# Kernel tuning notes

Measured on AMD Instinct MI355X. Metric: run time of the kernel, lower is better.

The kernel has to match this reference:

```python
import jax, jax.numpy as jnp
import numpy as np

N_NODES = 50000
N_EDGES = 800000
QRY = 128
KEY = 128
VAL = 128
HEADS = 8
HEAD_FEATS = VAL // HEADS
BN_EPS = 1e-5


def setup_inputs() -> dict:
    key = jax.random.key(0)
    ks = jax.random.split(key, 12)
    inp = {
        "ft_q": jax.random.normal(ks[0], (N_NODES, QRY), dtype=jnp.float32),
        "ft_k": jax.random.normal(ks[1], (N_NODES, KEY), dtype=jnp.float32),
        "src": jax.random.randint(ks[2], (N_EDGES,), 0, N_NODES, dtype=jnp.int32),
        "dst": jax.random.randint(ks[3], (N_EDGES,), 0, N_NODES, dtype=jnp.int32),
        # learned params
        "Wq": jax.random.normal(ks[4], (VAL, QRY), dtype=jnp.float32) / np.sqrt(QRY),
        "bq": jnp.zeros((VAL,), dtype=jnp.float32),
        "Wk": jax.random.normal(ks[5], (VAL, KEY), dtype=jnp.float32) / np.sqrt(KEY),
        "Wv": jax.random.normal(ks[6], (VAL, QRY), dtype=jnp.float32) / np.sqrt(QRY),
        "attn_e": jax.random.normal(ks[7], (VAL,), dtype=jnp.float32),
        "bn_q_g": jnp.ones((QRY,), dtype=jnp.float32),
        "bn_q_b": jnp.zeros((QRY,), dtype=jnp.float32),
        "bn_k_g": jnp.ones((KEY,), dtype=jnp.float32),
        "bn_k_b": jnp.zeros((KEY,), dtype=jnp.float32),
    }
    return inp


def _batch_norm(x, gamma, beta):
    # training-mode BatchNorm1d: normalize over batch dim
    mean = jnp.mean(x, axis=0, keepdims=True)
    var = jnp.var(x, axis=0, keepdims=True)
    return (x - mean) * jax.lax.rsqrt(var + BN_EPS) * gamma + beta


def reference(ft_q, ft_k, src, dst, Wq, bq, Wk, Wv, attn_e,
              bn_q_g, bn_q_b, bn_k_g, bn_k_b):
    ft_q = _batch_norm(ft_q, bn_q_g, bn_q_b)
    ft_k = _batch_norm(ft_k, bn_k_g, bn_k_b)

    q = ft_q @ Wq.T + bq                      # [N, VAL]
    k = ft_k @ Wk.T                           # [N, VAL]
    v = (ft_q @ Wv.T).reshape(-1, HEADS, HEAD_FEATS)  # [N, H, D]

    # u_add_v: per-edge e = q[src] + k[dst]
    e = q[src] + k[dst]                       # [E, VAL]
    e = (attn_e * jax.nn.sigmoid(e)).reshape(-1, HEADS, HEAD_FEATS).sum(-1)  # [E, H]

    # edge_softmax grouped by destination node
    m = jax.ops.segment_max(e, dst, num_segments=N_NODES)   # [N, H]
    ex = jnp.exp(e - m[dst])                                # [E, H]
    s = jax.ops.segment_sum(ex, dst, num_segments=N_NODES)  # [N, H]
    a = ex / s[dst]                                         # [E, H]

    # u_mul_e_sum: scatter-sum of v[src] * a over destination
    msg = v[src] * a[:, :, None]                            # [E, H, D]
    rst = jax.ops.segment_sum(msg, dst, num_segments=N_NODES)  # [N, H, D]
    return rst.reshape(-1, VAL)
```

## Files before the change

### kernel.cpp

```cpp
#include <hip/hip_runtime.h>

#define N_NODES 50000
#define N_EDGES 800000
#define FEATS 128
#define NCHUNK 196
#define CPAD 50176
#define GEMM_BX 196
#define GEMM_BLOCKS 588
#define SCAT_BLOCKS 3125
#define NTILE 782
#define NF_WAVES 8192

typedef __attribute__((ext_vector_type(8))) short bf16x8;
typedef __attribute__((ext_vector_type(4))) float f32x4;

__device__ __forceinline__ unsigned short f2bf(float f){
  unsigned u = __float_as_uint(f);
  u += 0x7FFF + ((u >> 16) & 1);
  return (unsigned short)(u >> 16);
}
__device__ __forceinline__ void unpack8(uint4 p, float* f){
  f[0]=__uint_as_float(p.x << 16); f[1]=__uint_as_float(p.x & 0xffff0000u);
  f[2]=__uint_as_float(p.y << 16); f[3]=__uint_as_float(p.y & 0xffff0000u);
  f[4]=__uint_as_float(p.z << 16); f[5]=__uint_as_float(p.z & 0xffff0000u);
  f[6]=__uint_as_float(p.w << 16); f[7]=__uint_as_float(p.w & 0xffff0000u);
}

__global__ __launch_bounds__(256) void stats_hist_kernel(
    const float* __restrict__ ftq, const float* __restrict__ ftk,
    float* __restrict__ sums, const int* __restrict__ dstE,
    int* __restrict__ counts, int* __restrict__ csums){
  __shared__ float red[4*FEATS];
  __shared__ int lchunk[NCHUNK];
  int tid = threadIdx.x, bid = blockIdx.x;
  if (bid < 768){
    for (int i = tid; i < 4*FEATS; i += 256) red[i] = 0.f;
    __syncthreads();
    int c = tid & 127, half = tid >> 7;
    float sq=0.f, qq=0.f, sk=0.f, kk2=0.f;
    for (int r = bid*2 + half; r < N_NODES; r += 1536){
      float xq = ftq[(size_t)r*FEATS + c];
      float xk = ftk[(size_t)r*FEATS + c];
      sq += xq; qq += xq*xq; sk += xk; kk2 += xk*xk;
    }
    atomicAdd(&red[0*FEATS+c], sq);
    atomicAdd(&red[1*FEATS+c], qq);
    atomicAdd(&red[2*FEATS+c], sk);
    atomicAdd(&red[3*FEATS+c], kk2);
    __syncthreads();
    if (tid < FEATS){
      atomicAdd(&sums[0*FEATS+tid], red[0*FEATS+tid]);
      atomicAdd(&sums[1*FEATS+tid], red[1*FEATS+tid]);
      atomicAdd(&sums[2*FEATS+tid], red[2*FEATS+tid]);
      atomicAdd(&sums[3*FEATS+tid], red[3*FEATS+tid]);
    }
  } else {
    for (int i = tid; i < NCHUNK; i += 256) lchunk[i] = 0;
    __syncthreads();
    for (int t = (bid-768)*256 + tid; t < N_EDGES; t += 256*256){
      int d = dstE[t];
      atomicAdd(&counts[d], 1);
      atomicAdd(&lchunk[d >> 8], 1);
    }
    __syncthreads();
    for (int i = tid; i < NCHUNK; i += 256)
      if (lchunk[i]) atomicAdd(&csums[i], lchunk[i]);
  }
}

__global__ __launch_bounds__(256) void scan_fold_kernel(
    const int* __restrict__ counts, const int* __restrict__ csums,
    int* __restrict__ loc, int* __restrict__ bscan,
    const float* __restrict__ Wq, const float* __restrict__ bq,
    const float* __restrict__ Wk, const float* __restrict__ Wv,
    const float* __restrict__ gq, const float* __restrict__ bqn,
    const float* __restrict__ gk, const float* __restrict__ bkn,
    const float* __restrict__ sums,
    unsigned short* __restrict__ Wb, float* __restrict__ bias){
  __shared__ int s[256];
  int tid = threadIdx.x, bid = blockIdx.x;
  if (bid < NCHUNK){
    int i = bid*256 + tid;
    int v = counts[i];
    s[tid] = v; __syncthreads();
    for (int d = 1; d < 256; d <<= 1){
      int tv = (tid >= d) ? s[tid-d] : 0; __syncthreads();
      s[tid] += tv; __syncthreads();
    }
    loc[i] = s[tid] - v;
  } else if (bid == NCHUNK){
    int v = (tid < NCHUNK) ? csums[tid] : 0;
    s[tid] = v; __syncthreads();
    for (int d = 1; d < 256; d <<= 1){
      int tv = (tid >= d) ? s[tid-d] : 0; __syncthreads();
      s[tid] += tv; __syncthreads();
    }
    if (tid < NCHUNK) bscan[tid] = s[tid] - v;
  } else {
    int wv = (bid - NCHUNK - 1)*4 + (tid >> 6);
    int lane = tid & 63;
    int m = wv >> 7;
    int o = wv & 127;
    const float* Wsrc = (m==0) ? Wq : (m==1) ? Wv : Wk;
    const float* g   = (m==2) ? gk : gq;
    const float* bb  = (m==2) ? bkn : bqn;
    const float* s0  = (m==2) ? (sums + 2*FEATS) : sums;
    const float invN = 1.0f / (float)N_NODES;
    float acc = 0.f;
    unsigned short w2[2];
    int i0 = lane*2;
    #pragma unroll
    for (int t = 0; t < 2; t++){
      int i = i0 + t;
      float mean = s0[i]*invN;
      float var  = s0[FEATS+i]*invN - mean*mean;
      float rstd = rsqrtf(var + 1e-5f);
      float scale = g[i]*rstd;
      float shift = bb[i] - mean*scale;
      float w = Wsrc[o*FEATS + i];
      w2[t] = f2bf(w*scale);
      acc += shift*w;
    }
    ((unsigned*)Wb)[(m*FEATS*FEATS + o*FEATS + i0) >> 1] =
        (unsigned)w2[0] | ((unsigned)w2[1] << 16);
    #pragma unroll
    for (int off = 1; off < 64; off <<= 1) acc += __shfl_xor(acc, off);
    if (lane == 0) bias[m*FEATS + o] = acc + ((m==0) ? bq[o] : 0.f);
  }
}

__global__ __launch_bounds__(256) void gemm_scatter_kernel(
    const float* __restrict__ ftq, const float* __restrict__ ftk,
    const unsigned short* __restrict__ Wball, const float* __restrict__ biasall,
    unsigned short* __restrict__ qv, unsigned short* __restrict__ kb,
    const int* __restrict__ dstE, const int* __restrict__ srcE,
    const int* __restrict__ loc, const int* __restrict__ bscan,
    int* __restrict__ cursor, int* __restrict__ src_csr){
  __shared__ unsigned short Bs[FEATS][136];
  int tid = threadIdx.x, bid = blockIdx.x;
  if (bid >= GEMM_BLOCKS){
    int t = (bid - GEMM_BLOCKS)*256 + tid;
    int d = dstE[t];
    int p = atomicAdd(&cursor[d], 1);
    src_csr[loc[d] + bscan[d >> 8] + p] = srcE[t];
    return;
  }
  int m = bid / GEMM_BX;
  int bx = bid - m*GEMM_BX;
  const float* X = (m==2) ? ftk : ftq;
  {
    const uint4* srcp = (const uint4*)(Wball + m*FEATS*FEATS);
    for (int idx = tid; idx < FEATS*FEATS/8; idx += 256){
      int n = idx >> 4;
      int kk = (idx & 15) * 8;
      *(uint4*)&Bs[n][kk] = srcp[idx];
    }
  }
  __syncthreads();
  int wave = tid >> 6, lane = tid & 63;
  int mrow = lane & 15, quad = lane >> 4;
  unsigned short* Out = (m==2) ? kb : (qv + m*128);
  const int ostride = (m==2) ? FEATS : 256;
  float bv[8];
  #pragma unroll
  for (int ct = 0; ct < 8; ct++) bv[ct] = biasall[m*FEATS + ct*16 + mrow];
  for (int t = bx; t < NTILE; t += GEMM_BX){
    int row0 = t*64;
    int arow = row0 + wave*16 + mrow;
    bool rok = arow < N_NODES;
    size_t abase = (size_t)(rok ? arow : 0) * FEATS;
    bf16x8 afrag[4];
    #pragma unroll
    for (int kt = 0; kt < 4; kt++){
      const float* xp = X + abase + kt*32 + quad*8;
      float4 x0 = *(const float4*)xp;
      float4 x1 = *(const float4*)(xp + 4);
      if (!rok){ x0 = make_float4(0.f,0.f,0.f,0.f); x1 = x0; }
      bf16x8 a;
      a[0]=(short)f2bf(x0.x); a[1]=(short)f2bf(x0.y); a[2]=(short)f2bf(x0.z); a[3]=(short)f2bf(x0.w);
      a[4]=(short)f2bf(x1.x); a[5]=(short)f2bf(x1.y); a[6]=(short)f2bf(x1.z); a[7]=(short)f2bf(x1.w);
      afrag[kt] = a;
    }
    f32x4 acc[8];
    #pragma unroll
    for (int i = 0; i < 8; i++) acc[i] = (f32x4){0.f,0.f,0.f,0.f};
    #pragma unroll
    for (int kt = 0; kt < 4; kt++){
      int kbk = kt*32 + quad*8;
      #pragma unroll
      for (int ct = 0; ct < 8; ct++){
        bf16x8 b = *(bf16x8*)&Bs[ct*16 + mrow][kbk];
        acc[ct] = __builtin_amdgcn_mfma_f32_16x16x32_bf16(afrag[kt], b, acc[ct], 0, 0, 0);
      }
    }
    #pragma unroll
    for (int ct = 0; ct < 8; ct++){
      int col = ct*16 + mrow;
      #pragma unroll
      for (int v = 0; v < 4; v++){
        int orow = row0 + wave*16 + quad*4 + v;
        unsigned ub = f2bf(acc[ct][v] + bv[ct]);
        unsigned partner = (unsigned)__shfl_xor((int)ub, 1);
        if (!(mrow & 1) && orow < N_NODES)
          *(unsigned*)&Out[(size_t)orow*ostride + col] = ub | (partner << 16);
      }
    }
  }
}

__global__ __launch_bounds__(256) void node_fused_kernel(
    const unsigned short* __restrict__ qv, const unsigned short* __restrict__ kb,
    const float* __restrict__ attn, const int* __restrict__ src_csr,
    const int* __restrict__ loc, const int* __restrict__ bscan,
    float* __restrict__ out){
  int tid = threadIdx.x;
  int lane = tid & 63;
  int h = lane & 7, g = lane >> 3;
  int w = blockIdx.x*4 + (tid >> 6);
  const float L2E = 1.44269504f;
  float ar[16];
  {
    const uint4* ap = (const uint4*)(attn + h*16);
    uint4 a0 = ap[0], a1 = ap[1], a2 = ap[2], a3 = ap[3];
    ar[0]=__uint_as_float(a0.x); ar[1]=__uint_as_float(a0.y); ar[2]=__uint_as_float(a0.z); ar[3]=__uint_as_float(a0.w);
    ar[4]=__uint_as_float(a1.x); ar[5]=__uint_as_float(a1.y); ar[6]=__uint_as_float(a1.z); ar[7]=__uint_as_float(a1.w);
    ar[8]=__uint_as_float(a2.x); ar[9]=__uint_as_float(a2.y); ar[10]=__uint_as_float(a2.z); ar[11]=__uint_as_float(a2.w);
    ar[12]=__uint_as_float(a3.x); ar[13]=__uint_as_float(a3.y); ar[14]=__uint_as_float(a3.z); ar[15]=__uint_as_float(a3.w);
  }
  for (int n = w; n < N_NODES; n += NF_WAVES){
    int off0 = loc[n]   + bscan[n>>8];
    int off1 = loc[n+1] + bscan[(n+1)>>8];
    int deg = off1 - off0;
    if (deg == 0){
      ((float2*)(out + (size_t)n*FEATS))[lane] = make_float2(0.f, 0.f);
      continue;
    }
    float kf2[16];
    {
      const unsigned short* kr = kb + (size_t)n*FEATS + h*16;
      uint4 k0 = *(const uint4*)kr;
      uint4 k1 = *(const uint4*)(kr + 8);
      float kf[16]; unpack8(k0, kf); unpack8(k1, kf+8);
      #pragma unroll
      for (int i = 0; i < 16; i++) kf2[i] = -L2E * kf[i];
    }
    float ssum = 0.f;
    float acc[16];
    #pragma unroll
    for (int i = 0; i < 16; i++) acc[i] = 0.f;
    int s_next = (g < deg) ? src_csr[off0 + g] : 0;
    for (int j = g; j < deg; j += 8){
      int s = s_next;
      if (j + 8 < deg) s_next = src_csr[off0 + j + 8];
      const unsigned short* qr = qv + (size_t)s*256 + h*16;
      uint4 q0 = *(const uint4*)qr;
      uint4 q1 = *(const uint4*)(qr + 8);
      uint4 v0 = *(const uint4*)(qr + 128);
      uint4 v1 = *(const uint4*)(qr + 136);
      float qf[16]; unpack8(q0, qf); unpack8(q1, qf+8);
      float t = 0.f;
      #pragma unroll
      for (int i = 0; i < 16; i++){
        float xs = fmaf(qf[i], -L2E, kf2[i]);
        float sg = __builtin_amdgcn_rcpf(1.f + __builtin_amdgcn_exp2f(xs));
        t = fmaf(ar[i], sg, t);
      }
      float ex = __builtin_amdgcn_exp2f(t * L2E);
      ssum += ex;
      float vf[16]; unpack8(v0, vf); unpack8(v1, vf+8);
      #pragma unroll
      for (int i = 0; i < 16; i++) acc[i] = fmaf(ex, vf[i], acc[i]);
    }
    ssum += __shfl_xor(ssum, 8); ssum += __shfl_xor(ssum, 16); ssum += __shfl_xor(ssum, 32);
    #pragma unroll
    for (int i = 0; i < 16; i++){
      acc[i] += __shfl_xor(acc[i], 8);
      acc[i] += __shfl_xor(acc[i], 16);
      acc[i] += __shfl_xor(acc[i], 32);
    }
    if (g == 0){
      float inv_s = 1.f / ssum;
      float4* op = (float4*)(out + (size_t)n*FEATS + h*16);
      op[0] = make_float4(acc[0]*inv_s, acc[1]*inv_s, acc[2]*inv_s, acc[3]*inv_s);
      op[1] = make_float4(acc[4]*inv_s, acc[5]*inv_s, acc[6]*inv_s, acc[7]*inv_s);
      op[2] = make_float4(acc[8]*inv_s, acc[9]*inv_s, acc[10]*inv_s, acc[11]*inv_s);
      op[3] = make_float4(acc[12]*inv_s, acc[13]*inv_s, acc[14]*inv_s, acc[15]*inv_s);
    }
  }
}

extern "C" void kernel_launch(void* const* d_in, const int* in_sizes, int n_in,
                              void* d_out, int out_size, void* d_ws, size_t ws_size,
                              hipStream_t stream){
  (void)in_sizes; (void)n_in; (void)out_size; (void)ws_size;
  const float* ftq  = (const float*)d_in[0];
  const float* ftk  = (const float*)d_in[1];
  const int*   srcE = (const int*)d_in[2];
  const int*   dstE = (const int*)d_in[3];
  const float* Wq   = (const float*)d_in[4];
  const float* bq   = (const float*)d_in[5];
  const float* Wk   = (const float*)d_in[6];
  const float* Wv   = (const float*)d_in[7];
  const float* attn = (const float*)d_in[8];
  const float* gq   = (const float*)d_in[9];
  const float* bqn  = (const float*)d_in[10];
  const float* gk   = (const float*)d_in[11];
  const float* bkn  = (const float*)d_in[12];

  char* ws = (char*)d_ws;
  int*   counts  = (int*)(ws + 0);
  int*   cursor  = (int*)(ws + 200704);
  float* sums    = (float*)(ws + 400704);
  int*   csums   = (int*)(ws + 402752);
  int*   loc     = (int*)(ws + 403536);
  int*   bscan   = (int*)(ws + 604240);
  int*   src_csr = (int*)(ws + 605024);
  unsigned short* Wb = (unsigned short*)(ws + 3805024);
  float* biasf   = (float*)(ws + 3903328);
  unsigned short* qv = (unsigned short*)(ws + 3904864);
  unsigned short* kb = qv + (size_t)N_NODES*256;
  float* out = (float*)d_out;

  hipMemsetAsync(ws, 0, 403536, stream);

  hipLaunchKernelGGL(stats_hist_kernel, dim3(1024), dim3(256), 0, stream,
                     ftq, ftk, sums, dstE, counts, csums);
  hipLaunchKernelGGL(scan_fold_kernel, dim3(293), dim3(256), 0, stream,
                     counts, csums, loc, bscan,
                     Wq, bq, Wk, Wv, gq, bqn, gk, bkn, sums, Wb, biasf);
  hipLaunchKernelGGL(gemm_scatter_kernel, dim3(GEMM_BLOCKS + SCAT_BLOCKS), dim3(256), 0, stream,
                     ftq, ftk, Wb, biasf, qv, kb, dstE, srcE, loc, bscan, cursor, src_csr);
  hipLaunchKernelGGL(node_fused_kernel, dim3(NF_WAVES/4), dim3(256), 0, stream,
                     qv, kb, attn, src_csr, loc, bscan, out);
}
```

Baseline: 290.0 us.

## Merge CSR offsets, share A tiles across Q/V GEMMs, unroll edge loop by two

Each scan block now computes its chunk base itself from csums, giving a single global offsets array in place of loc and bscan plus a separate block scan. The Q and V projections now share one set of loaded and converted A fragments per tile, with the weight tile restaged in shared memory between them, so ft_q is read once for both. The node kernel processes two edges per lane per iteration, issuing both gathers together for more memory-level parallelism. This replaces the prefetch-next-index scheme and adds register pressure.

```diff
diff --git a/kernel.cpp b/kernel.cpp
--- a/kernel.cpp
+++ b/kernel.cpp
@@ -5,7 +5,8 @@
 #define FEATS 128
 #define NCHUNK 196
 #define CPAD 50176
-#define GEMM_BX 196
+#define GEMM_QV 392
+#define GEMM_K 196
 #define GEMM_BLOCKS 588
 #define SCAT_BLOCKS 3125
 #define NTILE 782
@@ -70,7 +71,7 @@
 
 __global__ __launch_bounds__(256) void scan_fold_kernel(
     const int* __restrict__ counts, const int* __restrict__ csums,
-    int* __restrict__ loc, int* __restrict__ bscan,
+    int* __restrict__ offsets,
     const float* __restrict__ Wq, const float* __restrict__ bq,
     const float* __restrict__ Wk, const float* __restrict__ Wv,
     const float* __restrict__ gq, const float* __restrict__ bqn,
@@ -78,8 +79,19 @@
     const float* __restrict__ sums,
     unsigned short* __restrict__ Wb, float* __restrict__ bias){
   __shared__ int s[256];
+  __shared__ int sbase;
   int tid = threadIdx.x, bid = blockIdx.x;
   if (bid < NCHUNK){
+    s[tid] = (tid < bid) ? csums[tid] : 0;
+    __syncthreads();
+    for (int d = 128; d > 0; d >>= 1){
+      if (tid < d) s[tid] += s[tid + d];
+      __syncthreads();
+    }
+    if (tid == 0) sbase = s[0];
+    __syncthreads();
+    int base = sbase;
+    __syncthreads();
     int i = bid*256 + tid;
     int v = counts[i];
     s[tid] = v; __syncthreads();
@@ -87,17 +99,9 @@
       int tv = (tid >= d) ? s[tid-d] : 0; __syncthreads();
       s[tid] += tv; __syncthreads();
     }
-    loc[i] = s[tid] - v;
-  } else if (bid == NCHUNK){
-    int v = (tid < NCHUNK) ? csums[tid] : 0;
-    s[tid] = v; __syncthreads();
-    for (int d = 1; d < 256; d <<= 1){
-      int tv = (tid >= d) ? s[tid-d] : 0; __syncthreads();
-      s[tid] += tv; __syncthreads();
-    }
-    if (tid < NCHUNK) bscan[tid] = s[tid] - v;
+    offsets[i] = base + s[tid] - v;
   } else {
-    int wv = (bid - NCHUNK - 1)*4 + (tid >> 6);
+    int wv = (bid - NCHUNK)*4 + (tid >> 6);
     int lane = tid & 63;
     int m = wv >> 7;
     int o = wv & 127;
@@ -134,42 +138,26 @@
     const unsigned short* __restrict__ Wball, const float* __restrict__ biasall,
     unsigned short* __restrict__ qv, unsigned short* __restrict__ kb,
     const int* __restrict__ dstE, const int* __restrict__ srcE,
-    const int* __restrict__ loc, const int* __restrict__ bscan,
-    int* __restrict__ cursor, int* __restrict__ src_csr){
+    const int* __restrict__ offsets, int* __restrict__ cursor,
+    int* __restrict__ src_csr){
   __shared__ unsigned short Bs[FEATS][136];
   int tid = threadIdx.x, bid = blockIdx.x;
   if (bid >= GEMM_BLOCKS){
     int t = (bid - GEMM_BLOCKS)*256 + tid;
     int d = dstE[t];
     int p = atomicAdd(&cursor[d], 1);
-    src_csr[loc[d] + bscan[d >> 8] + p] = srcE[t];
+    src_csr[offsets[d] + p] = srcE[t];
     return;
   }
-  int m = bid / GEMM_BX;
-  int bx = bid - m*GEMM_BX;
-  const float* X = (m==2) ? ftk : ftq;
-  {
-    const uint4* srcp = (const uint4*)(Wball + m*FEATS*FEATS);
-    for (int idx = tid; idx < FEATS*FEATS/8; idx += 256){
-      int n = idx >> 4;
-      int kk = (idx & 15) * 8;
-      *(uint4*)&Bs[n][kk] = srcp[idx];
-    }
-  }
-  __syncthreads();
   int wave = tid >> 6, lane = tid & 63;
   int mrow = lane & 15, quad = lane >> 4;
-  unsigned short* Out = (m==2) ? kb : (qv + m*128);
-  const int ostride = (m==2) ? FEATS : 256;
-  float bv[8];
-  #pragma unroll
-  for (int ct = 0; ct < 8; ct++) bv[ct] = biasall[m*FEATS + ct*16 + mrow];
-  for (int t = bx; t < NTILE; t += GEMM_BX){
+
+  auto loadA = [&](int t, bf16x8* af){
     int row0 = t*64;
     int arow = row0 + wave*16 + mrow;
     bool rok = arow < N_NODES;
+    const float* X = (bid < GEMM_QV) ? ftq : ftk;
     size_t abase = (size_t)(rok ? arow : 0) * FEATS;
-    bf16x8 afrag[4];
     #pragma unroll
     for (int kt = 0; kt < 4; kt++){
       const float* xp = X + abase + kt*32 + quad*8;
@@ -179,8 +167,18 @@
       bf16x8 a;
       a[0]=(short)f2bf(x0.x); a[1]=(short)f2bf(x0.y); a[2]=(short)f2bf(x0.z); a[3]=(short)f2bf(x0.w);
       a[4]=(short)f2bf(x1.x); a[5]=(short)f2bf(x1.y); a[6]=(short)f2bf(x1.z); a[7]=(short)f2bf(x1.w);
-      afrag[kt] = a;
-    }
+      af[kt] = a;
+    }
+  };
+  auto stageB = [&](int m){
+    const uint4* srcp = (const uint4*)(Wball + m*FEATS*FEATS);
+    for (int idx = tid; idx < FEATS*FEATS/8; idx += 256){
+      int n = idx >> 4;
+      int kk = (idx & 15) * 8;
+      *(uint4*)&Bs[n][kk] = srcp[idx];
+    }
+  };
+  auto compute_store = [&](int t, const bf16x8* af, int m){
     f32x4 acc[8];
     #pragma unroll
     for (int i = 0; i < 8; i++) acc[i] = (f32x4){0.f,0.f,0.f,0.f};
@@ -190,29 +188,56 @@
       #pragma unroll
       for (int ct = 0; ct < 8; ct++){
         bf16x8 b = *(bf16x8*)&Bs[ct*16 + mrow][kbk];
-        acc[ct] = __builtin_amdgcn_mfma_f32_16x16x32_bf16(afrag[kt], b, acc[ct], 0, 0, 0);
+        acc[ct] = __builtin_amdgcn_mfma_f32_16x16x32_bf16(af[kt], b, acc[ct], 0, 0, 0);
       }
     }
+    unsigned short* Out = (m==2) ? kb : (qv + m*128);
+    const int ostride = (m==2) ? FEATS : 256;
+    int row0 = t*64;
     #pragma unroll
     for (int ct = 0; ct < 8; ct++){
       int col = ct*16 + mrow;
+      float bv = biasall[m*FEATS + col];
       #pragma unroll
       for (int v = 0; v < 4; v++){
         int orow = row0 + wave*16 + quad*4 + v;
-        unsigned ub = f2bf(acc[ct][v] + bv[ct]);
+        unsigned ub = f2bf(acc[ct][v] + bv);
         unsigned partner = (unsigned)__shfl_xor((int)ub, 1);
         if (!(mrow & 1) && orow < N_NODES)
           *(unsigned*)&Out[(size_t)orow*ostride + col] = ub | (partner << 16);
       }
     }
+  };
+
+  if (bid < GEMM_QV){
+    int t0 = bid, t1 = bid + GEMM_QV;
+    bf16x8 a0[4], a1[4];
+    stageB(0);
+    loadA(t0, a0); loadA(t1, a1);
+    __syncthreads();
+    compute_store(t0, a0, 0);
+    compute_store(t1, a1, 0);
+    __syncthreads();
+    stageB(1);
+    __syncthreads();
+    compute_store(t0, a0, 1);
+    compute_store(t1, a1, 1);
+  } else {
+    int bx = bid - GEMM_QV;
+    stageB(2);
+    __syncthreads();
+    bf16x8 af[4];
+    for (int t = bx; t < NTILE; t += GEMM_K){
+      loadA(t, af);
+      compute_store(t, af, 2);
+    }
   }
 }
 
 __global__ __launch_bounds__(256) void node_fused_kernel(
     const unsigned short* __restrict__ qv, const unsigned short* __restrict__ kb,
     const float* __restrict__ attn, const int* __restrict__ src_csr,
-    const int* __restrict__ loc, const int* __restrict__ bscan,
-    float* __restrict__ out){
+    const int* __restrict__ offsets, float* __restrict__ out){
   int tid = threadIdx.x;
   int lane = tid & 63;
   int h = lane & 7, g = lane >> 3;
@@ -228,9 +253,8 @@
     ar[12]=__uint_as_float(a3.x); ar[13]=__uint_as_float(a3.y); ar[14]=__uint_as_float(a3.z); ar[15]=__uint_as_float(a3.w);
   }
   for (int n = w; n < N_NODES; n += NF_WAVES){
-    int off0 = loc[n]   + bscan[n>>8];
-    int off1 = loc[n+1] + bscan[(n+1)>>8];
-    int deg = off1 - off0;
+    int off0 = offsets[n];
+    int deg = offsets[n+1] - off0;
     if (deg == 0){
       ((float2*)(out + (size_t)n*FEATS))[lane] = make_float2(0.f, 0.f);
       continue;
@@ -248,28 +272,45 @@
     float acc[16];
     #pragma unroll
     for (int i = 0; i < 16; i++) acc[i] = 0.f;
-    int s_next = (g < deg) ? src_csr[off0 + g] : 0;
-    for (int j = g; j < deg; j += 8){
-      int s = s_next;
-      if (j + 8 < deg) s_next = src_csr[off0 + j + 8];
-      const unsigned short* qr = qv + (size_t)s*256 + h*16;
-      uint4 q0 = *(const uint4*)qr;
-      uint4 q1 = *(const uint4*)(qr + 8);
-      uint4 v0 = *(const uint4*)(qr + 128);
-      uint4 v1 = *(const uint4*)(qr + 136);
-      float qf[16]; unpack8(q0, qf); unpack8(q1, qf+8);
-      float t = 0.f;
+    for (int j = g; j < deg; j += 16){
+      int j2 = j + 8;
+      bool has2 = j2 < deg;
+      int s1 = src_csr[off0 + j];
+      int s2 = has2 ? src_csr[off0 + j2] : s1;
+      const unsigned short* qr1 = qv + (size_t)s1*256 + h*16;
+      const unsigned short* qr2 = qv + (size_t)s2*256 + h*16;
+      uint4 q10 = *(const uint4*)qr1;
+      uint4 q11 = *(const uint4*)(qr1 + 8);
+      uint4 v10 = *(const uint4*)(qr1 + 128);
+      uint4 v11 = *(const uint4*)(qr1 + 136);
+      uint4 q20 = *(const uint4*)qr2;
+      uint4 q21 = *(const uint4*)(qr2 + 8);
+      uint4 v20 = *(const uint4*)(qr2 + 128);
+      uint4 v21 = *(const uint4*)(qr2 + 136);
+      float qf[16]; unpack8(q10, qf); unpack8(q11, qf+8);
+      float t1 = 0.f;
       #pragma unroll
       for (int i = 0; i < 16; i++){
         float xs = fmaf(qf[i], -L2E, kf2[i]);
         float sg = __builtin_amdgcn_rcpf(1.f + __builtin_amdgcn_exp2f(xs));
-        t = fmaf(ar[i], sg, t);
+        t1 = fmaf(ar[i], sg, t1);
       }
-      float ex = __builtin_amdgcn_exp2f(t * L2E);
-      ssum += ex;
-      float vf[16]; unpack8(v0, vf); unpack8(v1, vf+8);
-      #pragma unroll
-      for (int i = 0; i < 16; i++) acc[i] = fmaf(ex, vf[i], acc[i]);
+      float qg[16]; unpack8(q20, qg); unpack8(q21, qg+8);
+      float t2 = 0.f;
+      #pragma unroll
+      for (int i = 0; i < 16; i++){
+        float xs = fmaf(qg[i], -L2E, kf2[i]);
+        float sg = __builtin_amdgcn_rcpf(1.f + __builtin_amdgcn_exp2f(xs));
+        t2 = fmaf(ar[i], sg, t2);
+      }
+      float ex1 = __builtin_amdgcn_exp2f(t1 * L2E);
+      float ex2 = has2 ? __builtin_amdgcn_exp2f(t2 * L2E) : 0.f;
+      ssum += ex1 + ex2;
+      float vf[16]; unpack8(v10, vf); unpack8(v11, vf+8);
+      float vg[16]; unpack8(v20, vg); unpack8(v21, vg+8);
+      #pragma unroll
+      for (int i = 0; i < 16; i++)
+        acc[i] = fmaf(ex2, vg[i], fmaf(ex1, vf[i], acc[i]));
     }
     ssum += __shfl_xor(ssum, 8); ssum += __shfl_xor(ssum, 16); ssum += __shfl_xor(ssum, 32);
     #pragma unroll
@@ -312,12 +353,11 @@
   int*   cursor  = (int*)(ws + 200704);
   float* sums    = (float*)(ws + 400704);
   int*   csums   = (int*)(ws + 402752);
-  int*   loc     = (int*)(ws + 403536);
-  int*   bscan   = (int*)(ws + 604240);
-  int*   src_csr = (int*)(ws + 605024);
-  unsigned short* Wb = (unsigned short*)(ws + 3805024);
-  float* biasf   = (float*)(ws + 3903328);
-  unsigned short* qv = (unsigned short*)(ws + 3904864);
+  int*   offsets = (int*)(ws + 403536);
+  int*   src_csr = (int*)(ws + 604240);
+  unsigned short* Wb = (unsigned short*)(ws + 3804240);
+  float* biasf   = (float*)(ws + 3902544);
+  unsigned short* qv = (unsigned short*)(ws + 3904080);
   unsigned short* kb = qv + (size_t)N_NODES*256;
   float* out = (float*)d_out;
 
@@ -325,11 +365,11 @@
 
   hipLaunchKernelGGL(stats_hist_kernel, dim3(1024), dim3(256), 0, stream,
                      ftq, ftk, sums, dstE, counts, csums);
-  hipLaunchKernelGGL(scan_fold_kernel, dim3(293), dim3(256), 0, stream,
-                     counts, csums, loc, bscan,
+  hipLaunchKernelGGL(scan_fold_kernel, dim3(NCHUNK + 96), dim3(256), 0, stream,
+                     counts, csums, offsets,
                      Wq, bq, Wk, Wv, gq, bqn, gk, bkn, sums, Wb, biasf);
   hipLaunchKernelGGL(gemm_scatter_kernel, dim3(GEMM_BLOCKS + SCAT_BLOCKS), dim3(256), 0, stream,
-                     ftq, ftk, Wb, biasf, qv, kb, dstE, srcE, loc, bscan, cursor, src_csr);
+                     ftq, ftk, Wb, biasf, qv, kb, dstE, srcE, offsets, cursor, src_csr);
   hipLaunchKernelGGL(node_fused_kernel, dim3(NF_WAVES/4), dim3(256), 0, stream,
-                     qv, kb, attn, src_csr, loc, bscan, out);
-}
+                     qv, kb, attn, src_csr, offsets, out);
+}
```

New measurement: 297.3 us. 1.03x slower.
